# Performance work log

Measured on AMD Instinct MI355X. Metric: run time of the kernel, lower is better.

## Reference

```python
import jax, jax.numpy as jnp
import numpy as np

B, S, D = 4, 2048, 1024
H = 16
HD = D // H
FF = 4096
EPS = 1e-5

def _layernorm(x, g, b):
    mu = jnp.mean(x, axis=-1, keepdims=True)
    var = jnp.mean(jnp.square(x - mu), axis=-1, keepdims=True)
    return (x - mu) * jax.lax.rsqrt(var + EPS) * g + b

def setup_inputs() -> dict:
    key = jax.random.key(0)
    ks = jax.random.split(key, 12)
    s_attn = 1.0 / np.sqrt(D)
    s_ff1 = 1.0 / np.sqrt(D)
    s_ff2 = 1.0 / np.sqrt(FF)
    return {
        "x": jax.random.normal(ks[0], (B, S, D), jnp.float32),
        "ln1_g": jnp.ones((D,), jnp.float32),
        "ln1_b": jnp.zeros((D,), jnp.float32),
        "ln2_g": jnp.ones((D,), jnp.float32),
        "ln2_b": jnp.zeros((D,), jnp.float32),
        "Wq": jax.random.normal(ks[1], (D, D), jnp.float32) * s_attn,
        "Wk": jax.random.normal(ks[2], (D, D), jnp.float32) * s_attn,
        "Wv": jax.random.normal(ks[3], (D, D), jnp.float32) * s_attn,
        "Wo": jax.random.normal(ks[4], (D, D), jnp.float32) * s_attn,
        "W1": jax.random.normal(ks[5], (D, FF), jnp.float32) * s_ff1,
        "b1": jnp.zeros((FF,), jnp.float32),
        "W2": jax.random.normal(ks[6], (FF, D), jnp.float32) * s_ff2,
        "b2": jnp.zeros((D,), jnp.float32),
    }

def reference(x, ln1_g, ln1_b, ln2_g, ln2_b, Wq, Wk, Wv, Wo, W1, b1, W2, b2):
    # pre-LN self-attention (y = x), mask=None, dropout=0, attn proj bias=False
    h = _layernorm(x, ln1_g, ln1_b)                      # [B,S,D]
    q = (h @ Wq).reshape(B, S, H, HD).transpose(0, 2, 1, 3)  # [B,H,S,HD]
    k = (h @ Wk).reshape(B, S, H, HD).transpose(0, 2, 1, 3)
    v = (h @ Wv).reshape(B, S, H, HD).transpose(0, 2, 1, 3)
    scores = jnp.einsum('bhqd,bhkd->bhqk', q, k) / np.sqrt(HD)  # [B,H,S,S]
    attn = jax.nn.softmax(scores, axis=-1)
    o = jnp.einsum('bhqk,bhkd->bhqd', attn, v)           # [B,H,S,HD]
    o = o.transpose(0, 2, 1, 3).reshape(B, S, D) @ Wo
    x = x + o
    h2 = _layernorm(x, ln2_g, ln2_b)
    ff = jax.nn.relu(h2 @ W1 + b1) @ W2 + b2             # note: second FC also has relu per FC default
    ff = jax.nn.relu(ff)
    return x + ff
```

## Files before the change

### kernel.cpp

```cpp
#include <hip/hip_runtime.h>
#include <hip/hip_bf16.h>
#include <cstdint>
#include <cstddef>

typedef unsigned short u16;
typedef unsigned int u32;
typedef __bf16 bf16x2 __attribute__((ext_vector_type(2)));
typedef __bf16 bf16x8 __attribute__((ext_vector_type(8)));
typedef float f32x4 __attribute__((ext_vector_type(4)));

#define NB 4
#define NS 2048
#define ND 1024
#define NH 16
#define NHD 64
#define NFF 4096
#define CSC 0.18033688011112042f

#if __has_builtin(__builtin_amdgcn_exp2f)
#define EXP2(x) __builtin_amdgcn_exp2f(x)
#else
#define EXP2(x) exp2f(x)
#endif

__device__ __forceinline__ u16 f2b(float f) {
  union { bf16x2 h; u32 u; } v;
  v.h[0] = (__bf16)f; v.h[1] = (__bf16)f;
  return (u16)(v.u & 0xFFFF);
}
__device__ __forceinline__ u32 pack2(float a, float b) {
  union { bf16x2 h; u32 u; } v;
  v.h[0] = (__bf16)a; v.h[1] = (__bf16)b;
  return v.u;
}

__device__ __forceinline__ void async_copy16(const u16* g, u16* l) {
  __builtin_amdgcn_global_load_lds(
      (const __attribute__((address_space(1))) void*)(const void*)g,
      (__attribute__((address_space(3))) void*)(void*)l, 16, 0, 0);
}

__global__ __launch_bounds__(256) void transpose_f2b(const float* __restrict__ in,
                                                     u16* __restrict__ out,
                                                     int R, int C) {
  __shared__ float tile[32][33];
  const int bx = blockIdx.x * 32;
  const int by = blockIdx.y * 32;
  const int tx = threadIdx.x & 31, ty = threadIdx.x >> 5;
#pragma unroll
  for (int i = 0; i < 32; i += 8)
    tile[ty + i][tx] = in[(size_t)(by + ty + i) * C + bx + tx];
  __syncthreads();
#pragma unroll
  for (int i = 0; i < 32; i += 8)
    out[(size_t)(bx + ty + i) * R + by + tx] = f2b(tile[tx][ty + i]);
}

__global__ __launch_bounds__(256) void ln_kernel(const float* __restrict__ xin,
                                                 const float* __restrict__ g,
                                                 const float* __restrict__ b,
                                                 u16* __restrict__ out) {
  const int row = blockIdx.x;
  const int tid = threadIdx.x;
  const float* p = xin + (size_t)row * ND;
  float v[4];
#pragma unroll
  for (int i = 0; i < 4; i++) v[i] = p[tid + 256 * i];
  float s = 0.f, ss = 0.f;
#pragma unroll
  for (int i = 0; i < 4; i++) { s += v[i]; ss += v[i] * v[i]; }
  for (int off = 32; off > 0; off >>= 1) {
    s += __shfl_down(s, off);
    ss += __shfl_down(ss, off);
  }
  __shared__ float r0[4], r1[4];
  const int w = tid >> 6;
  if ((tid & 63) == 0) { r0[w] = s; r1[w] = ss; }
  __syncthreads();
  s = r0[0] + r0[1] + r0[2] + r0[3];
  ss = r1[0] + r1[1] + r1[2] + r1[3];
  const float mu = s * (1.f / ND);
  const float var = ss * (1.f / ND) - mu * mu;
  const float rstd = rsqrtf(var + 1e-5f);
  u16* o = out + (size_t)row * ND;
#pragma unroll
  for (int i = 0; i < 4; i++) {
    const int c = tid + 256 * i;
    o[c] = f2b((v[i] - mu) * rstd * g[c] + b[c]);
  }
}

template <int OUT_MODE, int RES_MODE, bool BIAS, bool RELU>
__global__ __launch_bounds__(256) void gemm_bt(const u16* __restrict__ A,
                                               const u16* __restrict__ Bt,
                                               const float* __restrict__ bias,
                                               const float* __restrict__ res,
                                               void* __restrict__ out,
                                               u16* __restrict__ outK,
                                               u16* __restrict__ outV,
                                               int M, int N, int K) {
  __shared__ __align__(16) u16 lA[128 * 64];
  __shared__ __align__(16) u16 lB[128 * 64];
  const int tid = threadIdx.x;
  const int bm = blockIdx.y * 128, bn = blockIdx.x * 128;
  const int w = tid >> 6, lane = tid & 63, quad = lane >> 4, l16 = lane & 15;
  const int wm = (w & 1) * 64, wn = (w >> 1) * 64;
  const int sw = l16 & 7;

  f32x4 acc[4][4];
#pragma unroll
  for (int i = 0; i < 4; i++)
#pragma unroll
    for (int j = 0; j < 4; j++) acc[i][j] = (f32x4){0.f, 0.f, 0.f, 0.f};

  const int srow = w * 8 + (lane >> 3);
  const int sch = (lane & 7) ^ ((lane >> 3) & 7);
  const u16* Ap = A + (size_t)(bm + srow) * K + sch * 8;
  const u16* Bp = Bt + (size_t)(bn + srow) * K + sch * 8;

  for (int k0 = 0; k0 < K; k0 += 64) {
    __syncthreads();
#pragma unroll
    for (int c = 0; c < 4; c++)
      async_copy16(Ap + (size_t)c * 32 * K + k0, &lA[(c * 32 + w * 8) * 64]);
#pragma unroll
    for (int c = 0; c < 4; c++)
      async_copy16(Bp + (size_t)c * 32 * K + k0, &lB[(c * 32 + w * 8) * 64]);
    __syncthreads();
#pragma unroll
    for (int x = 0; x < 2; x++) {
      bf16x8 af[4], bf[4];
#pragma unroll
      for (int i = 0; i < 4; i++)
        af[i] = *(const bf16x8*)&lA[(wm + i * 16 + l16) * 64 + ((x * 4 + quad) ^ sw) * 8];
#pragma unroll
      for (int j = 0; j < 4; j++)
        bf[j] = *(const bf16x8*)&lB[(wn + j * 16 + l16) * 64 + ((x * 4 + quad) ^ sw) * 8];
#pragma unroll
      for (int i = 0; i < 4; i++)
#pragma unroll
        for (int j = 0; j < 4; j++)
          acc[i][j] = __builtin_amdgcn_mfma_f32_16x16x32_bf16(af[i], bf[j], acc[i][j], 0, 0, 0);
    }
  }

  if constexpr (OUT_MODE == 3) {
    const int m0 = bm + wm;
#pragma unroll
    for (int i = 0; i < 4; i++) {
#pragma unroll
      for (int j = 0; j < 4; j++) {
        const int n = bn + wn + j * 16 + l16;
        const int mB = m0 + i * 16 + quad * 4;
        const int bb = mB >> 11, s = mB & 2047;
        if (bn < 1024) {
          const int hh = n >> 6, hd = n & 63;
          u16* o = (u16*)out + (((size_t)(bb * NH + hh) * NS + s) * NHD + hd);
#pragma unroll
          for (int r = 0; r < 4; r++) o[(size_t)r * NHD] = f2b(acc[i][j][r] * CSC);
        } else if (bn < 2048) {
          const int nk = n - 1024;
          const int hh = nk >> 6, hd = nk & 63;
          u16* o = outK + (((size_t)(bb * NH + hh) * NS + s) * NHD + hd);
#pragma unroll
          for (int r = 0; r < 4; r++) o[(size_t)r * NHD] = f2b(acc[i][j][r]);
        } else {
          const int nv = n - 2048;
          const int hh = nv >> 6, hd = nv & 63;
          uint2 pk = make_uint2(pack2(acc[i][j][0], acc[i][j][1]),
                                pack2(acc[i][j][2], acc[i][j][3]));
          *(uint2*)&outV[((size_t)(bb * NH + hh) * NHD + hd) * NS + s] = pk;
        }
      }
    }
  } else {
#pragma unroll
    for (int i = 0; i < 4; i++) {
#pragma unroll
      for (int r = 0; r < 4; r++) {
        const int m = bm + wm + i * 16 + quad * 4 + r;
#pragma unroll
        for (int j = 0; j < 4; j++) {
          const int n = bn + wn + j * 16 + l16;
          float vv = acc[i][j][r];
          if constexpr (BIAS) vv += bias[n];
          if constexpr (RELU) vv = fmaxf(vv, 0.f);
          if constexpr (RES_MODE == 1) vv += res[(size_t)m * N + n];
          if constexpr (OUT_MODE == 0) {
            ((u16*)out)[(size_t)m * N + n] = f2b(vv);
          } else {
            ((float*)out)[(size_t)m * N + n] = vv;
          }
        }
      }
    }
  }
}

#define OSTR 72
__global__ __launch_bounds__(256, 4) void attn_kernel(const u16* __restrict__ Q,
                                                      const u16* __restrict__ K,
                                                      const u16* __restrict__ VT,
                                                      u16* __restrict__ O) {
  __shared__ __align__(16) u16 lK[128 * 64];
  __shared__ __align__(16) u16 lV[64 * 128];
  const int tid = threadIdx.x;
  const int w = tid >> 6, lane = tid & 63, quad = lane >> 4, l16 = lane & 15;
  const int sw = l16 & 7;

  const int bid = blockIdx.x;
  const int xcd = bid & 7, slot = bid >> 3;
  const int bh = xcd + 8 * (slot >> 5);
  const int q0 = (slot & 31) * 64;
  const size_t base = (size_t)bh * NS * NHD;

  const u16* qrow = Q + base + (size_t)(q0 + w * 16 + l16) * NHD;
  bf16x8 qf[2];
  qf[0] = *(const bf16x8*)(qrow + quad * 8);
  qf[1] = *(const bf16x8*)(qrow + 32 + quad * 8);

  const int krow = w * 8 + (lane >> 3);
  const int kch = (lane & 7) ^ ((lane >> 3) & 7);
  const int vrow = w * 4 + (lane >> 4);
  const int vch = (lane & 15) ^ (vrow & 7);
  const u16* kp = K + base + (size_t)krow * 64 + kch * 8;
  const u16* vp = VT + base + (size_t)vrow * NS + vch * 8;

  float l_i = 0.f;
  f32x4 oa[4];
#pragma unroll
  for (int jo = 0; jo < 4; jo++) oa[jo] = (f32x4){0.f, 0.f, 0.f, 0.f};

  for (int kt = 0; kt < NS / 128; ++kt) {
    __syncthreads();
#pragma unroll
    for (int c = 0; c < 4; c++)
      async_copy16(kp + (size_t)c * 32 * 64, &lK[(c * 32 + w * 8) * 64]);
#pragma unroll
    for (int c = 0; c < 4; c++)
      async_copy16(vp + (size_t)c * 16 * NS, &lV[(c * 16 + w * 4) * 128]);
    __syncthreads();
    kp += 128 * 64;
    vp += 128;

    f32x4 sc[8];
#pragma unroll
    for (int j = 0; j < 8; j++) sc[j] = (f32x4){0.f, 0.f, 0.f, 0.f};
#pragma unroll
    for (int x = 0; x < 2; x++)
#pragma unroll
      for (int j = 0; j < 8; j++) {
        bf16x8 kf = *(const bf16x8*)&lK[(j * 16 + l16) * 64 + ((x * 4 + quad) ^ sw) * 8];
        sc[j] = __builtin_amdgcn_mfma_f32_16x16x32_bf16(kf, qf[x], sc[j], 0, 0, 0);
      }

    float rsum = 0.f;
#pragma unroll
    for (int j = 0; j < 8; j++) {
#pragma unroll
      for (int r = 0; r < 4; r++) sc[j][r] = EXP2(sc[j][r]);
      rsum += (sc[j][0] + sc[j][1]) + (sc[j][2] + sc[j][3]);
    }
    rsum += __shfl_xor(rsum, 16);
    rsum += __shfl_xor(rsum, 32);
    l_i += rsum;

#pragma unroll
    for (int x = 0; x < 4; x++) {
      u32 A0 = pack2(sc[2 * x][0], sc[2 * x][1]);
      u32 A1 = pack2(sc[2 * x][2], sc[2 * x][3]);
      u32 B0 = pack2(sc[2 * x + 1][0], sc[2 * x + 1][1]);
      u32 B1 = pack2(sc[2 * x + 1][2], sc[2 * x + 1][3]);
      asm("v_permlane32_swap_b32 %0, %1" : "+v"(A0), "+v"(B0));
      asm("v_permlane32_swap_b32 %0, %1" : "+v"(A1), "+v"(B1));
      asm("v_permlane16_swap_b32 %0, %1" : "+v"(A0), "+v"(B0));
      asm("v_permlane16_swap_b32 %0, %1" : "+v"(A1), "+v"(B1));
      union { u32 u[4]; bf16x8 h; } bq;
      bq.u[0] = A0; bq.u[1] = A1; bq.u[2] = B0; bq.u[3] = B1;
#pragma unroll
      for (int jo = 0; jo < 4; jo++) {
        bf16x8 av = *(const bf16x8*)&lV[(jo * 16 + l16) * 128 + ((x * 4 + quad) ^ sw) * 8];
        oa[jo] = __builtin_amdgcn_mfma_f32_16x16x32_bf16(av, bq.h, oa[jo], 0, 0, 0);
      }
    }
  }

  __syncthreads();
  const float inv = 1.f / l_i;
  u16* lo = &lK[w * 16 * OSTR];
#pragma unroll
  for (int jo = 0; jo < 4; jo++)
#pragma unroll
    for (int pr = 0; pr < 2; pr++)
      *(u32*)&lo[l16 * OSTR + jo * 16 + quad * 4 + pr * 2] =
          pack2(oa[jo][2 * pr] * inv, oa[jo][2 * pr + 1] * inv);

  const int bb = bh >> 4, hh = bh & 15;
#pragma unroll
  for (int t = 0; t < 2; t++) {
    const int row = t * 8 + (lane >> 3);
    const int seg = lane & 7;
    bf16x8 ov = *(const bf16x8*)&lo[row * OSTR + seg * 8];
    const int srow = q0 + w * 16 + row;
    *(int4*)&O[((size_t)bb * NS + srow) * ND + hh * 64 + seg * 8] = *(int4*)&ov;
  }
}

extern "C" void kernel_launch(void* const* d_in, const int* in_sizes, int n_in,
                              void* d_out, int out_size, void* d_ws, size_t ws_size,
                              hipStream_t stream) {
  (void)in_sizes; (void)n_in; (void)out_size; (void)ws_size;
  const float* x = (const float*)d_in[0];
  const float* ln1g = (const float*)d_in[1];
  const float* ln1b = (const float*)d_in[2];
  const float* ln2g = (const float*)d_in[3];
  const float* ln2b = (const float*)d_in[4];
  const float* Wq = (const float*)d_in[5];
  const float* Wk = (const float*)d_in[6];
  const float* Wv = (const float*)d_in[7];
  const float* Wo = (const float*)d_in[8];
  const float* W1 = (const float*)d_in[9];
  const float* b1 = (const float*)d_in[10];
  const float* W2 = (const float*)d_in[11];
  const float* b2 = (const float*)d_in[12];

  u16* ws = (u16*)d_ws;
  u16* h     = ws;
  u16* WqkvT = ws + (size_t)8  * 1048576;
  u16* WoT   = ws + (size_t)11 * 1048576;
  u16* W1T   = ws + (size_t)12 * 1048576;
  u16* W2T   = ws + (size_t)16 * 1048576;
  u16* qb    = ws + (size_t)20 * 1048576;
  u16* kb    = ws + (size_t)28 * 1048576;
  u16* vt    = ws + (size_t)36 * 1048576;
  u16* ob    = ws + (size_t)44 * 1048576;
  float* x2  = (float*)(ws + (size_t)52 * 1048576);
  u16* ff    = qb;
  u16* h2    = h;

  const int M = NB * NS;

  transpose_f2b<<<dim3(32, 32), 256, 0, stream>>>(Wq, WqkvT, ND, ND);
  transpose_f2b<<<dim3(32, 32), 256, 0, stream>>>(Wk, WqkvT + (size_t)1024 * 1024, ND, ND);
  transpose_f2b<<<dim3(32, 32), 256, 0, stream>>>(Wv, WqkvT + (size_t)2048 * 1024, ND, ND);
  transpose_f2b<<<dim3(32, 32), 256, 0, stream>>>(Wo, WoT, ND, ND);
  transpose_f2b<<<dim3(128, 32), 256, 0, stream>>>(W1, W1T, ND, NFF);
  transpose_f2b<<<dim3(32, 128), 256, 0, stream>>>(W2, W2T, NFF, ND);

  ln_kernel<<<M, 256, 0, stream>>>(x, ln1g, ln1b, h);

  gemm_bt<3, 0, false, false><<<dim3(24, 64), 256, 0, stream>>>(
      h, WqkvT, nullptr, nullptr, qb, kb, vt, M, 3072, ND);

  attn_kernel<<<dim3(2048), 256, 0, stream>>>(qb, kb, vt, ob);

  gemm_bt<2, 1, false, false><<<dim3(8, 64), 256, 0, stream>>>(
      ob, WoT, nullptr, x, x2, nullptr, nullptr, M, ND, ND);

  ln_kernel<<<M, 256, 0, stream>>>(x2, ln2g, ln2b, h2);

  gemm_bt<0, 0, true, true><<<dim3(32, 64), 256, 0, stream>>>(
      h2, W1T, b1, nullptr, ff, nullptr, nullptr, M, NFF, ND);

  gemm_bt<2, 1, true, true><<<dim3(8, 64), 256, 0, stream>>>(
      ff, W2T, b2, x2, d_out, nullptr, nullptr, M, ND, NFF);
}
```

Before: 507.8 us.

## Double-buffer LDS tiles in GEMM to prefetch next K-slice during MFMA

The GEMM now keeps two LDS buffers each for the A and B tiles. It issues the async global-to-LDS copies for the next K-tile before running the MFMAs on the current one, and drops one of the two barriers per iteration. The goal is to overlap global memory latency with matrix compute instead of stalling on each tile load. The cost is twice the shared memory per block (64KB), which can lower how many blocks fit on each CU.

```diff
diff --git a/kernel.cpp b/kernel.cpp
--- a/kernel.cpp
+++ b/kernel.cpp
@@ -99,8 +99,8 @@
                                                u16* __restrict__ outK,
                                                u16* __restrict__ outV,
                                                int M, int N, int K) {
-  __shared__ __align__(16) u16 lA[128 * 64];
-  __shared__ __align__(16) u16 lB[128 * 64];
+  __shared__ __align__(16) u16 lA[2][128 * 64];
+  __shared__ __align__(16) u16 lB[2][128 * 64];
   const int tid = threadIdx.x;
   const int bm = blockIdx.y * 128, bn = blockIdx.x * 128;
   const int w = tid >> 6, lane = tid & 63, quad = lane >> 4, l16 = lane & 15;
@@ -117,25 +117,40 @@
   const int sch = (lane & 7) ^ ((lane >> 3) & 7);
   const u16* Ap = A + (size_t)(bm + srow) * K + sch * 8;
   const u16* Bp = Bt + (size_t)(bn + srow) * K + sch * 8;
-
-  for (int k0 = 0; k0 < K; k0 += 64) {
+  const int NT = K >> 6;
+
+#pragma unroll
+  for (int c = 0; c < 4; c++)
+    async_copy16(Ap + (size_t)c * 32 * K, &lA[0][(c * 32 + w * 8) * 64]);
+#pragma unroll
+  for (int c = 0; c < 4; c++)
+    async_copy16(Bp + (size_t)c * 32 * K, &lB[0][(c * 32 + w * 8) * 64]);
+
+  for (int kt = 0; kt < NT; ++kt) {
+    const int cur = kt & 1;
     __syncthreads();
-#pragma unroll
-    for (int c = 0; c < 4; c++)
-      async_copy16(Ap + (size_t)c * 32 * K + k0, &lA[(c * 32 + w * 8) * 64]);
-#pragma unroll
-    for (int c = 0; c < 4; c++)
-      async_copy16(Bp + (size_t)c * 32 * K + k0, &lB[(c * 32 + w * 8) * 64]);
-    __syncthreads();
+    if (kt + 1 < NT) {
+      const size_t koff = (size_t)(kt + 1) * 64;
+#pragma unroll
+      for (int c = 0; c < 4; c++)
+        async_copy16(Ap + (size_t)c * 32 * K + koff,
+                     &lA[cur ^ 1][(c * 32 + w * 8) * 64]);
+#pragma unroll
+      for (int c = 0; c < 4; c++)
+        async_copy16(Bp + (size_t)c * 32 * K + koff,
+                     &lB[cur ^ 1][(c * 32 + w * 8) * 64]);
+    }
+    const u16* lAc = lA[cur];
+    const u16* lBc = lB[cur];
 #pragma unroll
     for (int x = 0; x < 2; x++) {
       bf16x8 af[4], bf[4];
 #pragma unroll
       for (int i = 0; i < 4; i++)
-        af[i] = *(const bf16x8*)&lA[(wm + i * 16 + l16) * 64 + ((x * 4 + quad) ^ sw) * 8];
+        af[i] = *(const bf16x8*)&lAc[(wm + i * 16 + l16) * 64 + ((x * 4 + quad) ^ sw) * 8];
 #pragma unroll
       for (int j = 0; j < 4; j++)
-        bf[j] = *(const bf16x8*)&lB[(wn + j * 16 + l16) * 64 + ((x * 4 + quad) ^ sw) * 8];
+        bf[j] = *(const bf16x8*)&lBc[(wn + j * 16 + l16) * 64 + ((x * 4 + quad) ^ sw) * 8];
 #pragma unroll
       for (int i = 0; i < 4; i++)
 #pragma unroll
```

Result: no change. 509.4 us (+0.3%).
